# Kernel optimization log

Measured on AMD Instinct MI355X. Metric: run time of the kernel, lower is better.

## Reference

```python
import jax, jax.numpy as jnp
import numpy as np

N_NODES = 50000
N_EDGES = 300000
D = 256
EPS = 1e-12


def setup_inputs() -> dict:
    key = jax.random.key(0)
    ks = jax.random.split(key, 10)
    h5_all = jax.random.normal(ks[0], (N_NODES, D), dtype=jnp.float32)
    edge_index = jax.random.randint(ks[1], (2, N_EDGES), 0, N_NODES, dtype=jnp.int64)
    edge_weight = jax.random.uniform(ks[2], (N_EDGES,), dtype=jnp.float32)
    s = 1.0 / np.sqrt(D)
    W6 = jax.random.normal(ks[3], (D, D), dtype=jnp.float32) * s
    b6 = jnp.zeros((D,), dtype=jnp.float32)
    W7 = jax.random.normal(ks[4], (D, D), dtype=jnp.float32) * s
    b7 = jnp.zeros((D,), dtype=jnp.float32)
    Wp = jax.random.normal(ks[5], (D, D), dtype=jnp.float32) * s
    bp = jnp.zeros((D,), dtype=jnp.float32)
    return {"h5_all": h5_all, "edge_index": edge_index, "edge_weight": edge_weight,
            "W6": W6, "b6": b6, "W7": W7, "b7": b7, "Wp": Wp, "bp": bp}


def _gcn_layer(x, W, b, src, dst, norm, n_nodes):
    # x: [N, D]; transform then gather-scale-scatter along edges
    xt = x @ W                                   # [N, D]
    msg = xt[src] * norm[:, None]                # [E, D] gathered + scaled
    agg = jax.ops.segment_sum(msg, dst, num_segments=n_nodes)  # [N, D]
    return jax.nn.relu(agg + b)


def reference(h5_all, edge_index, edge_weight, W6, b6, W7, b7, Wp, bp):
    src, dst = edge_index[0], edge_index[1]
    # symmetric degree normalization with edge weights (GCN-style)
    deg_out = jax.ops.segment_sum(edge_weight, src, num_segments=N_NODES)
    deg_in = jax.ops.segment_sum(edge_weight, dst, num_segments=N_NODES)
    norm = edge_weight * jax.lax.rsqrt(deg_out[src] * deg_in[dst] + EPS)  # [E]
    h6 = _gcn_layer(h5_all, W6, b6, src, dst, norm, N_NODES)
    h7 = _gcn_layer(h6, W7, b7, src, dst, norm, N_NODES)
    out = h7 @ Wp + bp                           # post_mp linear head
    return out
```

## Files before the change

kernel.cpp:

```cpp
#include <hip/hip_runtime.h>

#define N_NODES 50000
#define N_PANELS 3125
#define N_EDGES 300000
#define EPS_F 1e-12f
#define DEGB 64
#define WB 96
#define AB (N_NODES * 32 / 256)
#define FILLB 128
#define GB 512
#define SCAN_NB ((N_NODES + 255) / 256)
#define MASK48 ((1ull << 48) - 1)
#define ZBYTES (N_NODES * 20)

typedef _Float16 f16x8 __attribute__((ext_vector_type(8)));
typedef float f32x4 __attribute__((ext_vector_type(4)));

static __device__ inline f32x4 mfma_f16(f16x8 a, f16x8 b, f32x4 c) {
    return __builtin_amdgcn_mfma_f32_16x16x32_f16(a, b, c, 0, 0, 0);
}

static __device__ inline size_t swz(int row, int l) {
    return ((size_t)(row >> 4) * 8 + (l >> 2)) * 512 + (size_t)((l & 3) * 128 + (row & 15) * 8);
}


__global__ __launch_bounds__(256) void zero_kernel(int4* __restrict__ p, int n16) {
    int i = blockIdx.x * 256 + threadIdx.x;
    if (i < n16) p[i] = make_int4(0, 0, 0, 0);
}


__global__ __launch_bounds__(256) void p1_kernel(const int* __restrict__ ei,
                                                 const float* __restrict__ ew,
                                                 unsigned long long* __restrict__ pk_out,
                                                 unsigned long long* __restrict__ pk_in,
                                                 const float* __restrict__ W6,
                                                 const float* __restrict__ W7,
                                                 const float* __restrict__ Wp,
                                                 _Float16* __restrict__ Bsw,
                                                 const float* __restrict__ h5,
                                                 _Float16* __restrict__ Asw) {
    int b = blockIdx.x;
    if (b < DEGB) {
        for (int e = b * 256 + (int)threadIdx.x; e < N_EDGES; e += DEGB * 256) {
            int s = ei[e];
            int d = ei[N_EDGES + e];
            unsigned long long wfx = (unsigned long long)(ew[e] * 4294967296.0f);
            atomicAdd(&pk_out[s], wfx);
            atomicAdd(&pk_in[d], (1ull << 48) | wfx);
        }
    } else if (b < DEGB + WB) {
        int bb = b - DEGB;
        int wsel = bb >> 5;
        const float* W = (wsel == 0) ? W6 : (wsel == 1) ? W7 : Wp;
        int id = (bb & 31) * 256 + threadIdx.x;
        int n = id >> 5, l = id & 31;
        f16x8 o;
#pragma unroll
        for (int j = 0; j < 8; ++j)
            o[j] = (_Float16)W[(l * 8 + j) * 256 + n];
        *(f16x8*)&Bsw[(size_t)wsel * 65536 + swz(n, l)] = o;
    } else {
        int tid = (b - DEGB - WB) * 256 + threadIdx.x;
        int row = tid >> 5, l = tid & 31;
        const float* p = &h5[(size_t)row * 256 + l * 8];
        float4 v0 = *(const float4*)p;
        float4 v1 = *(const float4*)(p + 4);
        f16x8 o;
        o[0] = (_Float16)v0.x; o[1] = (_Float16)v0.y;
        o[2] = (_Float16)v0.z; o[3] = (_Float16)v0.w;
        o[4] = (_Float16)v1.x; o[5] = (_Float16)v1.y;
        o[6] = (_Float16)v1.z; o[7] = (_Float16)v1.w;
        *(f16x8*)&Asw[swz(row, l)] = o;
    }
}


__global__ __launch_bounds__(256) void scan1_kernel(const unsigned long long* __restrict__ pk_in,
                                                    const unsigned long long* __restrict__ pk_out,
                                                    float* __restrict__ deg_in,
                                                    float* __restrict__ deg_out,
                                                    int* __restrict__ partial) {
    __shared__ int sh[256];
    int i = blockIdx.x * 256 + threadIdx.x;
    int c = 0;
    if (i < N_NODES) {
        unsigned long long p = pk_in[i];
        c = (int)(p >> 48);
        deg_in[i] = (float)(p & MASK48) * 0x1p-32f;
        deg_out[i] = (float)pk_out[i] * 0x1p-32f;
    }
    sh[threadIdx.x] = c;
    __syncthreads();
    for (int off = 128; off > 0; off >>= 1) {
        if (threadIdx.x < (unsigned)off) sh[threadIdx.x] += sh[threadIdx.x + off];
        __syncthreads();
    }
    if (threadIdx.x == 0) partial[blockIdx.x] = sh[0];
}

__global__ __launch_bounds__(256) void scan23_kernel(const unsigned long long* __restrict__ pk_in,
                                                     const int* __restrict__ partial,
                                                     int* __restrict__ row_ptr) {
    __shared__ int ps[256];
    __shared__ int sh[256];
    int t = threadIdx.x;
    int pv = (t < SCAN_NB) ? partial[t] : 0;
    ps[t] = pv;
    __syncthreads();
    for (int off = 1; off < 256; off <<= 1) {
        int x = (t >= off) ? ps[t - off] : 0;
        __syncthreads();
        ps[t] += x;
        __syncthreads();
    }
    int incl = ps[t];
    __syncthreads();
    ps[t] = incl - pv;
    __syncthreads();
    const int boff = ps[blockIdx.x];

    int i = blockIdx.x * 256 + t;
    int v = (i < N_NODES) ? (int)(pk_in[i] >> 48) : 0;
    sh[t] = v;
    __syncthreads();
    for (int off = 1; off < 256; off <<= 1) {
        int x = (t >= off) ? sh[t - off] : 0;
        __syncthreads();
        sh[t] += x;
        __syncthreads();
    }
    if (i < N_NODES) row_ptr[i] = sh[t] - v + boff;
    if (i == 0) row_ptr[N_NODES] = N_EDGES;
}


__global__ __launch_bounds__(256) void p2_kernel(const int* __restrict__ ei,
                                                 const float* __restrict__ ew,
                                                 const float* __restrict__ deg_out,
                                                 const float* __restrict__ deg_in,
                                                 const int* __restrict__ row_ptr,
                                                 int* __restrict__ cur,
                                                 int2* __restrict__ csr,
                                                 const _Float16* __restrict__ Asw,
                                                 const _Float16* __restrict__ Bsw,
                                                 _Float16* __restrict__ xt) {
    __shared__ __align__(16) _Float16 ebuf[4][16 * 72];

    if (blockIdx.x < FILLB) {
        for (int e = blockIdx.x * 256 + (int)threadIdx.x; e < N_EDGES; e += FILLB * 256) {
            int s = ei[e];
            int d = ei[N_EDGES + e];
            float nm = ew[e] * rsqrtf(deg_out[s] * deg_in[d] + EPS_F);
            int pos = atomicAdd(&cur[d], 1);
            csr[row_ptr[d] + pos] = make_int2(s, __float_as_int(nm));
        }
        return;
    }

    const int t = threadIdx.x;
    const int w = t >> 6, lane = t & 63;

    f16x8 bf[4][8];
#pragma unroll
    for (int cp4 = 0; cp4 < 4; ++cp4)
#pragma unroll
        for (int kb = 0; kb < 8; ++kb)
            bf[cp4][kb] = *(const f16x8*)&Bsw[(size_t)((w * 4 + cp4) * 8 + kb) * 512 + lane * 8];

    for (int p = blockIdx.x - FILLB; p < N_PANELS; p += GB) {
        const _Float16* abase = &Asw[(size_t)p * 4096 + lane * 8];
        f16x8 af[8];
#pragma unroll
        for (int kb = 0; kb < 8; ++kb)
            af[kb] = *(const f16x8*)&abase[kb * 512];

        f32x4 acc[4];
#pragma unroll
        for (int cp4 = 0; cp4 < 4; ++cp4) acc[cp4] = (f32x4){0.f, 0.f, 0.f, 0.f};
#pragma unroll
        for (int kb = 0; kb < 8; ++kb)
#pragma unroll
            for (int cp4 = 0; cp4 < 4; ++cp4)
                acc[cp4] = mfma_f16(af[kb], bf[cp4][kb], acc[cp4]);

        _Float16* eb = ebuf[w];
        const int rq = 4 * (lane >> 4);
        const int lr = lane & 15;
#pragma unroll
        for (int cp4 = 0; cp4 < 4; ++cp4)
#pragma unroll
            for (int rr = 0; rr < 4; ++rr)
                eb[(rq + rr) * 72 + cp4 * 16 + lr] = (_Float16)acc[cp4][rr];
#pragma unroll
        for (int it = 0; it < 2; ++it) {
            int rl = it * 8 + (lane >> 3);
            f16x8 v = *(const f16x8*)&eb[rl * 72 + (lane & 7) * 8];
            *(f16x8*)&xt[(size_t)(p * 16 + rl) * 256 + w * 64 + (lane & 7) * 8] = v;
        }
    }
}


template <int MODE>
__global__ __launch_bounds__(256) void gemm_f16(const _Float16* __restrict__ Asw,
                                                const _Float16* __restrict__ Bsw,
                                                const float* __restrict__ bias,
                                                void* __restrict__ Cout) {
    __shared__ __align__(16) char ebraw[4][16 * 68 * 4];

    const int t = threadIdx.x;
    const int w = t >> 6, lane = t & 63;
    const int lr = lane & 15;

    f16x8 bf[4][8];
#pragma unroll
    for (int cp4 = 0; cp4 < 4; ++cp4)
#pragma unroll
        for (int kb = 0; kb < 8; ++kb)
            bf[cp4][kb] = *(const f16x8*)&Bsw[(size_t)((w * 4 + cp4) * 8 + kb) * 512 + lane * 8];

    float bc[4];
    if (MODE == 1) {
#pragma unroll
        for (int cp4 = 0; cp4 < 4; ++cp4) bc[cp4] = bias[w * 64 + cp4 * 16 + lr];
    }

    for (int p = blockIdx.x; p < N_PANELS; p += GB) {
        const _Float16* abase = &Asw[(size_t)p * 4096 + lane * 8];
        f16x8 af[8];
#pragma unroll
        for (int kb = 0; kb < 8; ++kb)
            af[kb] = *(const f16x8*)&abase[kb * 512];

        f32x4 acc[4];
#pragma unroll
        for (int cp4 = 0; cp4 < 4; ++cp4) acc[cp4] = (f32x4){0.f, 0.f, 0.f, 0.f};
#pragma unroll
        for (int kb = 0; kb < 8; ++kb)
#pragma unroll
            for (int cp4 = 0; cp4 < 4; ++cp4)
                acc[cp4] = mfma_f16(af[kb], bf[cp4][kb], acc[cp4]);

        const int rq = 4 * (lane >> 4);
        if (MODE == 0) {
            _Float16* eb = (_Float16*)ebraw[w];
#pragma unroll
            for (int cp4 = 0; cp4 < 4; ++cp4)
#pragma unroll
                for (int rr = 0; rr < 4; ++rr)
                    eb[(rq + rr) * 72 + cp4 * 16 + lr] = (_Float16)acc[cp4][rr];
            _Float16* xp = (_Float16*)Cout;
#pragma unroll
            for (int it = 0; it < 2; ++it) {
                int rl = it * 8 + (lane >> 3);
                f16x8 v = *(const f16x8*)&eb[rl * 72 + (lane & 7) * 8];
                *(f16x8*)&xp[(size_t)(p * 16 + rl) * 256 + w * 64 + (lane & 7) * 8] = v;
            }
        } else {
            float* eb = (float*)ebraw[w];
#pragma unroll
            for (int cp4 = 0; cp4 < 4; ++cp4)
#pragma unroll
                for (int rr = 0; rr < 4; ++rr)
                    eb[(rq + rr) * 68 + cp4 * 16 + lr] = acc[cp4][rr] + bc[cp4];
            float* op = (float*)Cout;
#pragma unroll
            for (int it = 0; it < 4; ++it) {
                int rl = it * 4 + (lane >> 4);
                float4 v = *(const float4*)&eb[rl * 68 + lr * 4];
                *(float4*)&op[(size_t)(p * 16 + rl) * 256 + w * 64 + lr * 4] = v;
            }
        }
    }
}


__global__ __launch_bounds__(256) void agg_kernel(const _Float16* __restrict__ xt,
                                                  const int* __restrict__ row_ptr,
                                                  const int2* __restrict__ csr,
                                                  const float* __restrict__ bias,
                                                  _Float16* __restrict__ Asw) {
    const int g = threadIdx.x >> 5;
    const int l = threadIdx.x & 31;
    const int v = blockIdx.x * 8 + g;
    const int d0 = l * 8;

    const int s0 = row_ptr[v];
    const int s1 = row_ptr[v + 1];

    float acc[8] = {0.f, 0.f, 0.f, 0.f, 0.f, 0.f, 0.f, 0.f};

    int i = s0;
    for (; i + 4 <= s1; i += 4) {
        int2 hd[4];
#pragma unroll
        for (int u = 0; u < 4; ++u) hd[u] = csr[i + u];
        f16x8 val[4];
#pragma unroll
        for (int u = 0; u < 4; ++u)
            val[u] = *(const f16x8*)&xt[(size_t)hd[u].x * 256 + d0];
#pragma unroll
        for (int u = 0; u < 4; ++u) {
            float wv = __int_as_float(hd[u].y);
#pragma unroll
            for (int j = 0; j < 8; ++j)
                acc[j] += (float)val[u][j] * wv;
        }
    }
    {
        int rem = s1 - i;
        int2 hd[3];
#pragma unroll
        for (int u = 0; u < 3; ++u)
            hd[u] = (u < rem) ? csr[i + u] : make_int2(0, 0);
        f16x8 val[3];
#pragma unroll
        for (int u = 0; u < 3; ++u)
            val[u] = *(const f16x8*)&xt[(size_t)hd[u].x * 256 + d0];
#pragma unroll
        for (int u = 0; u < 3; ++u) {
            float wv = __int_as_float(hd[u].y);
#pragma unroll
            for (int j = 0; j < 8; ++j)
                acc[j] += (float)val[u][j] * wv;
        }
    }

    f16x8 o;
#pragma unroll
    for (int j = 0; j < 8; ++j) {
        float r = acc[j] + bias[d0 + j];
        r = r > 0.f ? r : 0.f;
        o[j] = (_Float16)r;
    }
    *(f16x8*)&Asw[swz(v, l)] = o;
}


extern "C" void kernel_launch(void* const* d_in, const int* in_sizes, int n_in,
                              void* d_out, int out_size, void* d_ws, size_t ws_size,
                              hipStream_t stream) {
    (void)in_sizes; (void)n_in; (void)out_size; (void)ws_size;
    const float* h5 = (const float*)d_in[0];
    const int*   ei = (const int*)d_in[1];
    const float* ew = (const float*)d_in[2];
    const float* W6 = (const float*)d_in[3];
    const float* b6 = (const float*)d_in[4];
    const float* W7 = (const float*)d_in[5];
    const float* b7 = (const float*)d_in[6];
    const float* Wp = (const float*)d_in[7];
    const float* bp = (const float*)d_in[8];
    float* out = (float*)d_out;

    char* ws = (char*)d_ws;
    size_t off = 0;
    auto alloc = [&](size_t bytes) -> void* {
        void* p = ws + off;
        off = (off + bytes + 255) & ~(size_t)255;
        return p;
    };

    char* zblk = (char*)alloc(ZBYTES);
    unsigned long long* pk_out = (unsigned long long*)zblk;
    unsigned long long* pk_in  = (unsigned long long*)(zblk + N_NODES * 8);
    int* cur = (int*)(zblk + N_NODES * 16);

    float* deg_out = (float*)alloc(N_NODES * 4);
    float* deg_in  = (float*)alloc(N_NODES * 4);
    int*   row_ptr = (int*)alloc((N_NODES + 1) * 4);
    int*   partial = (int*)alloc(SCAN_NB * 4);
    int2*  csr     = (int2*)alloc(N_EDGES * 8);
    _Float16* Bsw  = (_Float16*)alloc(3 * 65536 * 2);
    _Float16* Asw  = (_Float16*)alloc((size_t)N_NODES * 256 * 2);
    _Float16* xt   = (_Float16*)alloc((size_t)N_NODES * 256 * 2);

    const int Z16 = ZBYTES / 16;

    zero_kernel<<<(Z16 + 255) / 256, 256, 0, stream>>>((int4*)zblk, Z16);

    p1_kernel<<<DEGB + WB + AB, 256, 0, stream>>>(ei, ew, pk_out, pk_in,
                                                  W6, W7, Wp, Bsw, h5, Asw);

    scan1_kernel<<<SCAN_NB, 256, 0, stream>>>(pk_in, pk_out, deg_in, deg_out, partial);
    scan23_kernel<<<SCAN_NB, 256, 0, stream>>>(pk_in, partial, row_ptr);

    p2_kernel<<<FILLB + GB, 256, 0, stream>>>(ei, ew, deg_out, deg_in, row_ptr, cur, csr,
                                              Asw, Bsw, xt);

    agg_kernel<<<N_NODES / 8, 256, 0, stream>>>(xt, row_ptr, csr, b6, Asw);
    gemm_f16<0><<<GB, 256, 0, stream>>>(Asw, Bsw + 65536, nullptr, xt);
    agg_kernel<<<N_NODES / 8, 256, 0, stream>>>(xt, row_ptr, csr, b7, Asw);
    gemm_f16<1><<<GB, 256, 0, stream>>>(Asw, Bsw + 2 * 65536, bp, out);
}
```

Before: 162.4 us.

## Fuse edge aggregation into following GEMM and shrink degree atomics to 32-bit

```diff
diff --git a/kernel.cpp b/kernel.cpp
--- a/kernel.cpp
+++ b/kernel.cpp
@@ -10,8 +10,7 @@
 #define FILLB 128
 #define GB 512
 #define SCAN_NB ((N_NODES + 255) / 256)
-#define MASK48 ((1ull << 48) - 1)
-#define ZBYTES (N_NODES * 20)
+#define ZBYTES (N_NODES * 12)
 
 typedef _Float16 f16x8 __attribute__((ext_vector_type(8)));
 typedef float f32x4 __attribute__((ext_vector_type(4)));
@@ -33,8 +32,8 @@
 
 __global__ __launch_bounds__(256) void p1_kernel(const int* __restrict__ ei,
                                                  const float* __restrict__ ew,
-                                                 unsigned long long* __restrict__ pk_out,
-                                                 unsigned long long* __restrict__ pk_in,
+                                                 unsigned* __restrict__ pk_out,
+                                                 unsigned* __restrict__ pk_in,
                                                  const float* __restrict__ W6,
                                                  const float* __restrict__ W7,
                                                  const float* __restrict__ Wp,
@@ -46,9 +45,9 @@
         for (int e = b * 256 + (int)threadIdx.x; e < N_EDGES; e += DEGB * 256) {
             int s = ei[e];
             int d = ei[N_EDGES + e];
-            unsigned long long wfx = (unsigned long long)(ew[e] * 4294967296.0f);
+            unsigned wfx = (unsigned)(ew[e] * 262144.0f);
             atomicAdd(&pk_out[s], wfx);
-            atomicAdd(&pk_in[d], (1ull << 48) | wfx);
+            atomicAdd(&pk_in[d], (1u << 24) | wfx);
         }
     } else if (b < DEGB + WB) {
         int bb = b - DEGB;
@@ -77,8 +76,8 @@
 }
 
 
-__global__ __launch_bounds__(256) void scan1_kernel(const unsigned long long* __restrict__ pk_in,
-                                                    const unsigned long long* __restrict__ pk_out,
+__global__ __launch_bounds__(256) void scan1_kernel(const unsigned* __restrict__ pk_in,
+                                                    const unsigned* __restrict__ pk_out,
                                                     float* __restrict__ deg_in,
                                                     float* __restrict__ deg_out,
                                                     int* __restrict__ partial) {
@@ -86,10 +85,10 @@
     int i = blockIdx.x * 256 + threadIdx.x;
     int c = 0;
     if (i < N_NODES) {
-        unsigned long long p = pk_in[i];
-        c = (int)(p >> 48);
-        deg_in[i] = (float)(p & MASK48) * 0x1p-32f;
-        deg_out[i] = (float)pk_out[i] * 0x1p-32f;
+        unsigned p = pk_in[i];
+        c = (int)(p >> 24);
+        deg_in[i] = (float)(p & 0xFFFFFFu) * 0x1p-18f;
+        deg_out[i] = (float)pk_out[i] * 0x1p-18f;
     }
     sh[threadIdx.x] = c;
     __syncthreads();
@@ -100,7 +99,7 @@
     if (threadIdx.x == 0) partial[blockIdx.x] = sh[0];
 }
 
-__global__ __launch_bounds__(256) void scan23_kernel(const unsigned long long* __restrict__ pk_in,
+__global__ __launch_bounds__(256) void scan23_kernel(const unsigned* __restrict__ pk_in,
                                                      const int* __restrict__ partial,
                                                      int* __restrict__ row_ptr) {
     __shared__ int ps[256];
@@ -122,7 +121,7 @@
     const int boff = ps[blockIdx.x];
 
     int i = blockIdx.x * 256 + t;
-    int v = (i < N_NODES) ? (int)(pk_in[i] >> 48) : 0;
+    int v = (i < N_NODES) ? (int)(pk_in[i] >> 24) : 0;
     sh[t] = v;
     __syncthreads();
     for (int off = 1; off < 256; off <<= 1) {
@@ -204,15 +203,21 @@
 
 
 template <int MODE>
-__global__ __launch_bounds__(256) void gemm_f16(const _Float16* __restrict__ Asw,
-                                                const _Float16* __restrict__ Bsw,
-                                                const float* __restrict__ bias,
-                                                void* __restrict__ Cout) {
+__global__ __launch_bounds__(256) void aggemm_kernel(const _Float16* __restrict__ xt,
+                                                     const int* __restrict__ row_ptr,
+                                                     const int2* __restrict__ csr,
+                                                     const float* __restrict__ bias_agg,
+                                                     const _Float16* __restrict__ Bsw,
+                                                     const float* __restrict__ bias_head,
+                                                     void* __restrict__ Cout) {
+    __shared__ __align__(16) _Float16 atile[16 * 264];
     __shared__ __align__(16) char ebraw[4][16 * 68 * 4];
 
     const int t = threadIdx.x;
     const int w = t >> 6, lane = t & 63;
     const int lr = lane & 15;
+    const int ar = t >> 4;
+    const int d0 = (t & 15) * 16;
 
     f16x8 bf[4][8];
 #pragma unroll
@@ -224,24 +229,86 @@
     float bc[4];
     if (MODE == 1) {
 #pragma unroll
-        for (int cp4 = 0; cp4 < 4; ++cp4) bc[cp4] = bias[w * 64 + cp4 * 16 + lr];
+        for (int cp4 = 0; cp4 < 4; ++cp4) bc[cp4] = bias_head[w * 64 + cp4 * 16 + lr];
+    }
+
+    float bgs[16];
+#pragma unroll
+    for (int q = 0; q < 4; ++q) {
+        float4 v = *(const float4*)&bias_agg[d0 + q * 4];
+        bgs[q * 4 + 0] = v.x; bgs[q * 4 + 1] = v.y;
+        bgs[q * 4 + 2] = v.z; bgs[q * 4 + 3] = v.w;
     }
 
     for (int p = blockIdx.x; p < N_PANELS; p += GB) {
-        const _Float16* abase = &Asw[(size_t)p * 4096 + lane * 8];
-        f16x8 af[8];
-#pragma unroll
-        for (int kb = 0; kb < 8; ++kb)
-            af[kb] = *(const f16x8*)&abase[kb * 512];
-
-        f32x4 acc[4];
-#pragma unroll
-        for (int cp4 = 0; cp4 < 4; ++cp4) acc[cp4] = (f32x4){0.f, 0.f, 0.f, 0.f};
+        const int v = p * 16 + ar;
+        const int s0 = row_ptr[v];
+        const int s1 = row_ptr[v + 1];
+        float acc[16];
+#pragma unroll
+        for (int j = 0; j < 16; ++j) acc[j] = 0.f;
+
+        int i = s0;
+        for (; i + 2 <= s1; i += 2) {
+            int2 h0 = csr[i], h1 = csr[i + 1];
+            f16x8 a0 = *(const f16x8*)&xt[(size_t)h0.x * 256 + d0];
+            f16x8 a1 = *(const f16x8*)&xt[(size_t)h0.x * 256 + d0 + 8];
+            f16x8 b0 = *(const f16x8*)&xt[(size_t)h1.x * 256 + d0];
+            f16x8 b1 = *(const f16x8*)&xt[(size_t)h1.x * 256 + d0 + 8];
+            float w0 = __int_as_float(h0.y);
+            float w1 = __int_as_float(h1.y);
+#pragma unroll
+            for (int j = 0; j < 8; ++j) {
+                acc[j]     += (float)a0[j] * w0;
+                acc[8 + j] += (float)a1[j] * w0;
+            }
+#pragma unroll
+            for (int j = 0; j < 8; ++j) {
+                acc[j]     += (float)b0[j] * w1;
+                acc[8 + j] += (float)b1[j] * w1;
+            }
+        }
+        if (i < s1) {
+            int2 h0 = csr[i];
+            f16x8 a0 = *(const f16x8*)&xt[(size_t)h0.x * 256 + d0];
+            f16x8 a1 = *(const f16x8*)&xt[(size_t)h0.x * 256 + d0 + 8];
+            float w0 = __int_as_float(h0.y);
+#pragma unroll
+            for (int j = 0; j < 8; ++j) {
+                acc[j]     += (float)a0[j] * w0;
+                acc[8 + j] += (float)a1[j] * w0;
+            }
+        }
+
+        f16x8 o0, o1;
+#pragma unroll
+        for (int j = 0; j < 8; ++j) {
+            float r0 = acc[j] + bgs[j];
+            float r1 = acc[8 + j] + bgs[8 + j];
+            r0 = r0 > 0.f ? r0 : 0.f;
+            r1 = r1 > 0.f ? r1 : 0.f;
+            o0[j] = (_Float16)r0;
+            o1[j] = (_Float16)r1;
+        }
+
+        __syncthreads();
+        *(f16x8*)&atile[ar * 264 + d0] = o0;
+        *(f16x8*)&atile[ar * 264 + d0 + 8] = o1;
+        __syncthreads();
+
+        f16x8 afr[8];
+#pragma unroll
+        for (int kb = 0; kb < 8; ++kb)
+            afr[kb] = *(const f16x8*)&atile[lr * 264 + kb * 32 + (lane >> 4) * 8];
+
+        f32x4 acc2[4];
+#pragma unroll
+        for (int cp4 = 0; cp4 < 4; ++cp4) acc2[cp4] = (f32x4){0.f, 0.f, 0.f, 0.f};
 #pragma unroll
         for (int kb = 0; kb < 8; ++kb)
 #pragma unroll
             for (int cp4 = 0; cp4 < 4; ++cp4)
-                acc[cp4] = mfma_f16(af[kb], bf[cp4][kb], acc[cp4]);
+                acc2[cp4] = mfma_f16(afr[kb], bf[cp4][kb], acc2[cp4]);
 
         const int rq = 4 * (lane >> 4);
         if (MODE == 0) {
@@ -250,13 +317,13 @@
             for (int cp4 = 0; cp4 < 4; ++cp4)
 #pragma unroll
                 for (int rr = 0; rr < 4; ++rr)
-                    eb[(rq + rr) * 72 + cp4 * 16 + lr] = (_Float16)acc[cp4][rr];
+                    eb[(rq + rr) * 72 + cp4 * 16 + lr] = (_Float16)acc2[cp4][rr];
             _Float16* xp = (_Float16*)Cout;
 #pragma unroll
             for (int it = 0; it < 2; ++it) {
                 int rl = it * 8 + (lane >> 3);
-                f16x8 v = *(const f16x8*)&eb[rl * 72 + (lane & 7) * 8];
-                *(f16x8*)&xp[(size_t)(p * 16 + rl) * 256 + w * 64 + (lane & 7) * 8] = v;
+                f16x8 vv = *(const f16x8*)&eb[rl * 72 + (lane & 7) * 8];
+                *(f16x8*)&xp[(size_t)(p * 16 + rl) * 256 + w * 64 + (lane & 7) * 8] = vv;
             }
         } else {
             float* eb = (float*)ebraw[w];
@@ -264,78 +331,16 @@
             for (int cp4 = 0; cp4 < 4; ++cp4)
 #pragma unroll
                 for (int rr = 0; rr < 4; ++rr)
-                    eb[(rq + rr) * 68 + cp4 * 16 + lr] = acc[cp4][rr] + bc[cp4];
+                    eb[(rq + rr) * 68 + cp4 * 16 + lr] = acc2[cp4][rr] + bc[cp4];
             float* op = (float*)Cout;
 #pragma unroll
             for (int it = 0; it < 4; ++it) {
                 int rl = it * 4 + (lane >> 4);
-                float4 v = *(const float4*)&eb[rl * 68 + lr * 4];
-                *(float4*)&op[(size_t)(p * 16 + rl) * 256 + w * 64 + lr * 4] = v;
+                float4 vv = *(const float4*)&eb[rl * 68 + lr * 4];
+                *(float4*)&op[(size_t)(p * 16 + rl) * 256 + w * 64 + lr * 4] = vv;
             }
         }
     }
-}
-
-
-__global__ __launch_bounds__(256) void agg_kernel(const _Float16* __restrict__ xt,
-                                                  const int* __restrict__ row_ptr,
-                                                  const int2* __restrict__ csr,
-                                                  const float* __restrict__ bias,
-                                                  _Float16* __restrict__ Asw) {
-    const int g = threadIdx.x >> 5;
-    const int l = threadIdx.x & 31;
-    const int v = blockIdx.x * 8 + g;
-    const int d0 = l * 8;
-
-    const int s0 = row_ptr[v];
-    const int s1 = row_ptr[v + 1];
-
-    float acc[8] = {0.f, 0.f, 0.f, 0.f, 0.f, 0.f, 0.f, 0.f};
-
-    int i = s0;
-    for (; i + 4 <= s1; i += 4) {
-        int2 hd[4];
-#pragma unroll
-        for (int u = 0; u < 4; ++u) hd[u] = csr[i + u];
-        f16x8 val[4];
-#pragma unroll
-        for (int u = 0; u < 4; ++u)
-            val[u] = *(const f16x8*)&xt[(size_t)hd[u].x * 256 + d0];
-#pragma unroll
-        for (int u = 0; u < 4; ++u) {
-            float wv = __int_as_float(hd[u].y);
-#pragma unroll
-            for (int j = 0; j < 8; ++j)
-                acc[j] += (float)val[u][j] * wv;
-        }
-    }
-    {
-        int rem = s1 - i;
-        int2 hd[3];
-#pragma unroll
-        for (int u = 0; u < 3; ++u)
-            hd[u] = (u < rem) ? csr[i + u] : make_int2(0, 0);
-        f16x8 val[3];
-#pragma unroll
-        for (int u = 0; u < 3; ++u)
-            val[u] = *(const f16x8*)&xt[(size_t)hd[u].x * 256 + d0];
-#pragma unroll
-        for (int u = 0; u < 3; ++u) {
-            float wv = __int_as_float(hd[u].y);
-#pragma unroll
-            for (int j = 0; j < 8; ++j)
-                acc[j] += (float)val[u][j] * wv;
-        }
-    }
-
-    f16x8 o;
-#pragma unroll
-    for (int j = 0; j < 8; ++j) {
-        float r = acc[j] + bias[d0 + j];
-        r = r > 0.f ? r : 0.f;
-        o[j] = (_Float16)r;
-    }
-    *(f16x8*)&Asw[swz(v, l)] = o;
 }
 
 
@@ -363,9 +368,9 @@
     };
 
     char* zblk = (char*)alloc(ZBYTES);
-    unsigned long long* pk_out = (unsigned long long*)zblk;
-    unsigned long long* pk_in  = (unsigned long long*)(zblk + N_NODES * 8);
-    int* cur = (int*)(zblk + N_NODES * 16);
+    unsigned* pk_out = (unsigned*)zblk;
+    unsigned* pk_in  = (unsigned*)(zblk + N_NODES * 4);
+    int* cur = (int*)(zblk + N_NODES * 8);
 
     float* deg_out = (float*)alloc(N_NODES * 4);
     float* deg_in  = (float*)alloc(N_NODES * 4);
@@ -389,8 +394,9 @@
     p2_kernel<<<FILLB + GB, 256, 0, stream>>>(ei, ew, deg_out, deg_in, row_ptr, cur, csr,
                                               Asw, Bsw, xt);
 
-    agg_kernel<<<N_NODES / 8, 256, 0, stream>>>(xt, row_ptr, csr, b6, Asw);
-    gemm_f16<0><<<GB, 256, 0, stream>>>(Asw, Bsw + 65536, nullptr, xt);
-    agg_kernel<<<N_NODES / 8, 256, 0, stream>>>(xt, row_ptr, csr, b7, Asw);
-    gemm_f16<1><<<GB, 256, 0, stream>>>(Asw, Bsw + 2 * 65536, bp, out);
-}
+    aggemm_kernel<0><<<GB, 256, 0, stream>>>(xt, row_ptr, csr, b6, Bsw + 65536,
+                                             nullptr, Asw);
+
+    aggemm_kernel<1><<<GB, 256, 0, stream>>>(Asw, row_ptr, csr, b7, Bsw + 2 * 65536,
+                                             bp, out);
+}
```

Measured after the change: 166.6 us. +2.6%, slower.
